# Kernel tuning notes

Hardware: AMD Instinct MI355X
Metric: run time of the kernel (lower is better)

## Reference

```python
import jax, jax.numpy as jnp
import numpy as np

B, S, D = 1, 2048, 1024
H, DH = 16, 64
FF_INNER = 4 * D          # 4096
FUSED = 2 * FF_INNER      # 8192
ROT_BASE = 1000.0


def _rope_tables(seq_len, dim_head):
    # rotarizer: inv_freq = (base ** (arange(0, dh, 2)/dh)) ** -1 ; cached in bfloat16
    inv_freq = 1.0 / (ROT_BASE ** (jnp.arange(0, dim_head, 2, dtype=jnp.float32) / dim_head))
    t = jnp.arange(seq_len, dtype=jnp.float32)
    freqs = jnp.outer(t, inv_freq)                     # [S, DH/2]
    cos = jnp.cos(freqs).astype(jnp.bfloat16)[None, :, None, :]  # [1,S,1,DH/2]
    sin = jnp.sin(freqs).astype(jnp.bfloat16)[None, :, None, :]
    return cos, sin


def _apply_rope(x, cos, sin):
    d = x.shape[-1] // 2
    x1, x2 = x[..., :d], x[..., d:]
    y1 = x1 * cos + x2 * sin
    y2 = -x1 * sin + x2 * cos
    return jnp.concatenate([y1, y2], axis=-1).astype(x.dtype)


def _l2norm(x):
    # F.normalize(p=2, dim=-1), eps=1e-12
    n = jnp.linalg.norm(x, axis=-1, keepdims=True)
    return x / jnp.maximum(n, 1e-12)


def setup_inputs() -> dict:
    key = jax.random.key(0)
    ks = jax.random.split(key, 12)
    std = 0.02
    inp = {
        "h_states": jax.random.normal(ks[0], (B, S, D), jnp.float32),
        "Wq": jax.random.normal(ks[1], (D, D), jnp.float32) * std,
        "Wk": jax.random.normal(ks[2], (D, D), jnp.float32) * std,
        "Wv": jax.random.normal(ks[3], (D, D), jnp.float32) * std,
        "Wqb": jax.random.normal(ks[4], (D, D), jnp.float32) * std,
        "Wkb": jax.random.normal(ks[5], (D, D), jnp.float32) * std,
        "Wo": jax.random.normal(ks[6], (D, D), jnp.float32) * std,
        "bo": jnp.zeros((D,), jnp.float32),
        "W1": jax.random.normal(ks[7], (D, FUSED), jnp.float32) * std,
        "b1": jnp.zeros((FUSED,), jnp.float32),
        "W2": jax.random.normal(ks[8], (FF_INNER, D), jnp.float32) * std,
        "b2": jnp.zeros((D,), jnp.float32),
        "learnedlambda": jnp.asarray(1.0, jnp.float32),
        # l2normscale init: log(S^2 - S) for training_seqlen S
        "l2normscale": jnp.asarray(np.log(float(S) ** 2 - float(S)), np.float32),
    }
    return inp


def reference(h_states, Wq, Wk, Wv, Wqb, Wkb, Wo, bo, W1, b1, W2, b2, learnedlambda, l2normscale):
    b, s, d = h_states.shape
    scale = DH ** -0.5

    # layerwisenorm: RMSNorm, no affine
    eps = jnp.finfo(h_states.dtype).eps
    x = h_states * jax.lax.rsqrt(jnp.mean(jnp.square(h_states), axis=-1, keepdims=True) + eps)

    # projections -> [B,S,H,DH]
    def proj(W):
        return (x @ W).reshape(b, s, H, DH)
    q, k, v = proj(Wq), proj(Wk), proj(Wv)
    qb, kb = proj(Wqb), proj(Wkb)

    cos, sin = _rope_tables(s, DH)
    # per-head qk-norm (l2norm) then rope; v untouched
    q = _apply_rope(_l2norm(q), cos, sin)
    k = _apply_rope(_l2norm(k), cos, sin)
    qb = _apply_rope(_l2norm(qb), cos, sin)
    kb = _apply_rope(_l2norm(kb), cos, sin)

    causal = jnp.tril(jnp.ones((s, s), bool))  # [S,S]

    # main attention: scale=1 (l2norm path), causal softmax, scaled by l2normscale
    scores = jnp.einsum("bqhd,bkhd->bhqk", q, k)
    scores = jnp.where(causal[None, None], scores, -jnp.inf)
    attn = jax.nn.softmax(scores, axis=-1)
    y = l2normscale * jnp.einsum("bhqk,bkhd->bhqd", attn, v)  # [B,H,S,DH]

    # bias attention: masked raw scores @ ones == causal row-sum, broadcast over DH
    sb = jnp.einsum("bqhd,bkhd->bhqk", qb, kb) * scale
    sb = jnp.where(causal[None, None], sb, 0.0)
    y = y + jnp.sum(sb, axis=-1, keepdims=True)  # broadcast over head dim

    y = y.transpose(0, 2, 1, 3).reshape(b, s, d)
    attn_out = y @ Wo + bo

    # fused SwiGLU: chunk -> (x_part, gate); silu(gate) * x_part
    u = x @ W1 + b1
    xp, gate = u[..., :FF_INNER], u[..., FF_INNER:]
    ff = (jax.nn.silu(gate) * xp) @ W2 + b2

    return h_states * learnedlambda + ff + attn_out
```

## Files before the change

kernel.cpp:

```cpp
#include <hip/hip_runtime.h>
#include <hip/hip_bf16.h>
#include <math.h>

typedef __bf16 bf16x8 __attribute__((ext_vector_type(8)));
typedef float  f32x4  __attribute__((ext_vector_type(4)));

#define GLD16(g, l) __builtin_amdgcn_global_load_lds(                      \
    (const __attribute__((address_space(1))) void*)(g),                    \
    (__attribute__((address_space(3))) void*)(l), 16, 0, 0)

#define SCHED_FENCE() __builtin_amdgcn_sched_barrier(0)


__global__ __launch_bounds__(256) void repack_k(
    const float* __restrict__ Wq, const float* __restrict__ Wk,
    const float* __restrict__ Wv, const float* __restrict__ Wqb,
    const float* __restrict__ Wkb, const float* __restrict__ Wo,
    const float* __restrict__ W2, const float* __restrict__ W1,
    __bf16* __restrict__ Wt5, __bf16* __restrict__ WoW2t,
    __bf16* __restrict__ W1t) {
  int t = blockIdx.x;
  const float* in; __bf16* outp;
  int ldin, ldout, r0, c0, cin0, oofs;
  if (t < 5120) {
    int w = t >> 10, rem = t & 1023;
    const float* src[5] = {Wq, Wk, Wv, Wqb, Wkb};
    in = src[w]; ldin = 1024;
    r0 = (rem >> 5) << 5; c0 = (rem & 31) << 5; cin0 = c0;
    outp = Wt5 + (size_t)w * 1048576; ldout = 1024; oofs = 0;
  } else if (t < 6144) {
    int rem = t - 5120;
    in = Wo; ldin = 1024;
    r0 = (rem >> 5) << 5; c0 = (rem & 31) << 5; cin0 = c0;
    outp = WoW2t; ldout = 5120; oofs = 0;
  } else if (t < 10240) {
    int rem = t - 6144;
    in = W2; ldin = 1024;
    r0 = (rem >> 5) << 5; c0 = (rem & 31) << 5; cin0 = c0;
    outp = WoW2t; ldout = 5120; oofs = 1024;
  } else {
    int rem = t - 10240;
    in = W1; ldin = 8192;
    c0 = (rem & 255) << 5; r0 = (rem >> 8) << 5;
    cin0 = ((c0 >> 5) & 1) * 4096 + (c0 >> 6) * 32;
    outp = W1t; ldout = 1024; oofs = 0;
  }
  __shared__ float sh[32][33];
  int tid = threadIdx.x, tx = tid & 31, ty = tid >> 5;
  #pragma unroll
  for (int i = ty; i < 32; i += 8)
    sh[i][tx] = in[(size_t)(r0 + i) * ldin + cin0 + tx];
  __syncthreads();
  #pragma unroll
  for (int i = ty; i < 32; i += 8)
    outp[(size_t)(c0 + i) * ldout + oofs + r0 + tx] = (__bf16)sh[tx][i];
}

__global__ __launch_bounds__(256) void tconv_k(const float* __restrict__ in,
                                               __bf16* __restrict__ out,
                                               int ldin, int ldout) {
  __shared__ float t[32][33];
  int r0 = blockIdx.y * 32, c0 = blockIdx.x * 32;
  int tid = threadIdx.x, tx = tid & 31, ty = tid >> 5;
  #pragma unroll
  for (int i = ty; i < 32; i += 8)
    t[i][tx] = in[(size_t)(r0 + i) * ldin + c0 + tx];
  __syncthreads();
  #pragma unroll
  for (int i = ty; i < 32; i += 8)
    out[(size_t)(c0 + i) * ldout + r0 + tx] = (__bf16)t[tx][i];
}

__global__ __launch_bounds__(256) void rmsnorm_k(const float* __restrict__ hs,
                                                 __bf16* __restrict__ x) {
  int row = blockIdx.x, tid = threadIdx.x;
  const float4 v = ((const float4*)(hs + (size_t)row * 1024))[tid];
  float ss = v.x * v.x + v.y * v.y + v.z * v.z + v.w * v.w;
  #pragma unroll
  for (int o = 32; o > 0; o >>= 1) ss += __shfl_xor(ss, o);
  __shared__ float ps[4];
  if ((tid & 63) == 0) ps[tid >> 6] = ss;
  __syncthreads();
  float tot = ps[0] + ps[1] + ps[2] + ps[3];
  float r = rsqrtf(tot * (1.0f / 1024.0f) + 1.1920929e-7f);
  __bf16* xr = x + (size_t)row * 1024 + tid * 4;
  xr[0] = (__bf16)(v.x * r); xr[1] = (__bf16)(v.y * r);
  xr[2] = (__bf16)(v.z * r); xr[3] = (__bf16)(v.w * r);
}

__global__ __launch_bounds__(256, 3) void gemm_qkv_k(
    const __bf16* __restrict__ A, const __bf16* __restrict__ Bt,
    __bf16* __restrict__ qbf, __bf16* __restrict__ kbf,
    float* __restrict__ qb32, float* __restrict__ kb32,
    float* __restrict__ vproj) {
  const int K = 1024;
  __shared__ __bf16 sA[3][128 * 32];
  __shared__ __bf16 sB[3][128 * 32];
  const int tid = threadIdx.x;
  const int lane = tid & 63;
  const int quad = lane >> 4, l16 = lane & 15;
  const int wave = tid >> 6;
  const int waveM = wave >> 1, waveN = wave & 1;
  const int m0 = blockIdx.y * 128, n0 = blockIdx.x * 128;
  const int nk = K >> 5;
  const int rowS = tid >> 2;
  const int kg = ((tid & 3) ^ ((rowS >> 1) & 3)) * 8;
  const __bf16* gA0 = A + (size_t)(m0 + rowS) * K + kg;
  const __bf16* gA1 = gA0 + (size_t)64 * K;
  const __bf16* gB0 = Bt + (size_t)(n0 + rowS) * K + kg;
  const __bf16* gB1 = gB0 + (size_t)64 * K;
  const int lo0 = tid * 8, lo1 = 2048 + tid * 8;

  auto stage = [&](int t) {
    int s = t % 3;
    __bf16* dA = sA[s];
    __bf16* dB = sB[s];
    GLD16(gA0 + t * 32, dA + lo0);
    GLD16(gA1 + t * 32, dA + lo1);
    GLD16(gB0 + t * 32, dB + lo0);
    GLD16(gB1 + t * 32, dB + lo1);
  };
  stage(0); stage(1);

  f32x4 acc[4][4] = {};
  #pragma unroll 1
  for (int i = 0; i < nk; ++i) {
    if (i < nk - 1)
      asm volatile("s_waitcnt vmcnt(4)" ::: "memory");
    else
      asm volatile("s_waitcnt vmcnt(0)" ::: "memory");
    __builtin_amdgcn_s_barrier();
    SCHED_FENCE();
    int cs = i % 3;
    const __bf16* cA = sA[cs];
    const __bf16* cB = sB[cs];
    if (i + 2 < nk) stage(i + 2);
    SCHED_FENCE();
    bf16x8 af[4], bfv[4];
    #pragma unroll
    for (int mt = 0; mt < 4; ++mt) {
      int r = waveM * 64 + mt * 16 + l16;
      af[mt] = *(const bf16x8*)(cA + r * 32 + ((quad ^ ((r >> 1) & 3)) * 8));
    }
    #pragma unroll
    for (int nt = 0; nt < 4; ++nt) {
      int r = waveN * 64 + nt * 16 + l16;
      bfv[nt] = *(const bf16x8*)(cB + r * 32 + ((quad ^ ((r >> 1) & 3)) * 8));
    }
    __builtin_amdgcn_s_setprio(1);
    #pragma unroll
    for (int mt = 0; mt < 4; ++mt)
      #pragma unroll
      for (int nt = 0; nt < 4; ++nt)
        acc[mt][nt] = __builtin_amdgcn_mfma_f32_16x16x32_bf16(af[mt], bfv[nt], acc[mt][nt], 0, 0, 0);
    __builtin_amdgcn_s_setprio(0);
    SCHED_FENCE();
  }

  const int wid = n0 >> 10;
  const int cw0 = (n0 & 1023) + waveN * 64;
  if (wid == 2) {
    #pragma unroll
    for (int mt = 0; mt < 4; ++mt) {
      int row = m0 + waveM * 64 + mt * 16 + quad * 4;
      #pragma unroll
      for (int nt = 0; nt < 4; ++nt) {
        int col = cw0 + nt * 16 + l16;
        #pragma unroll
        for (int r = 0; r < 4; ++r)
          vproj[(size_t)(row + r) * 1024 + col] = acc[mt][nt][r];
      }
    }
  } else {
    const float inv0 = exp2f(-0.31143076f * (float)l16);
    const float inv1 = exp2f(-0.31143076f * (float)(16 + l16));
    #pragma unroll
    for (int mt = 0; mt < 4; ++mt) {
      #pragma unroll
      for (int r = 0; r < 4; ++r) {
        int srow = m0 + waveM * 64 + mt * 16 + quad * 4 + r;
        float a0 = acc[mt][0][r], a1 = acc[mt][1][r];
        float a2 = acc[mt][2][r], a3 = acc[mt][3][r];
        float ss = a0 * a0 + a1 * a1 + a2 * a2 + a3 * a3;
        ss += __shfl_xor(ss, 1); ss += __shfl_xor(ss, 2);
        ss += __shfl_xor(ss, 4); ss += __shfl_xor(ss, 8);
        float yn = 1.0f / fmaxf(sqrtf(ss), 1e-12f);
        float ang0 = (float)srow * inv0;
        float cb0 = (float)(__bf16)__cosf(ang0);
        float sb0 = (float)(__bf16)__sinf(ang0);
        float ang1 = (float)srow * inv1;
        float cb1 = (float)(__bf16)__cosf(ang1);
        float sb1 = (float)(__bf16)__sinf(ang1);
        float y0 = a0 * yn, y1 = a1 * yn, y2 = a2 * yn, y3 = a3 * yn;
        float o0 =  y0 * cb0 + y2 * sb0;
        float o1 =  y1 * cb1 + y3 * sb1;
        float o2 = -y0 * sb0 + y2 * cb0;
        float o3 = -y1 * sb1 + y3 * cb1;
        size_t base = (size_t)srow * 1024 + cw0 + l16;
        if (wid == 0) {
          qbf[base]      = (__bf16)o0; qbf[base + 16] = (__bf16)o1;
          qbf[base + 32] = (__bf16)o2; qbf[base + 48] = (__bf16)o3;
        } else if (wid == 1) {
          kbf[base]      = (__bf16)o0; kbf[base + 16] = (__bf16)o1;
          kbf[base + 32] = (__bf16)o2; kbf[base + 48] = (__bf16)o3;
        } else if (wid == 3) {
          qb32[base]      = o0; qb32[base + 16] = o1;
          qb32[base + 32] = o2; qb32[base + 48] = o3;
        } else {
          kb32[base]      = o0; kb32[base + 16] = o1;
          kb32[base + 32] = o2; kb32[base + 48] = o3;
        }
      }
    }
  }
}

__global__ __launch_bounds__(256, 3) void gemm_partk_k(
    const __bf16* __restrict__ A, const __bf16* __restrict__ Bt,
    float* __restrict__ P, int N, int K) {
  __shared__ __bf16 sA[3][128 * 32];
  __shared__ __bf16 sB[3][128 * 32];
  const int tid = threadIdx.x;
  const int lane = tid & 63;
  const int quad = lane >> 4, l16 = lane & 15;
  const int wave = tid >> 6;
  const int waveM = wave >> 1, waveN = wave & 1;
  const int m0 = blockIdx.y * 128, n0 = blockIdx.x * 128;
  const int kz = blockIdx.z, nz = gridDim.z;
  const int kper = K / nz, kbeg = kz * kper;
  const int nk = kper >> 5;
  const size_t MN = (size_t)gridDim.y * 128 * N;
  float* C = P + (size_t)kz * MN;
  const int rowS = tid >> 2;
  const int kg = ((tid & 3) ^ ((rowS >> 1) & 3)) * 8;
  const __bf16* gA0 = A + (size_t)(m0 + rowS) * K + kbeg + kg;
  const __bf16* gA1 = gA0 + (size_t)64 * K;
  const __bf16* gB0 = Bt + (size_t)(n0 + rowS) * K + kbeg + kg;
  const __bf16* gB1 = gB0 + (size_t)64 * K;
  const int lo0 = tid * 8, lo1 = 2048 + tid * 8;

  auto stage = [&](int t) {
    int s = t % 3;
    __bf16* dA = sA[s];
    __bf16* dB = sB[s];
    GLD16(gA0 + t * 32, dA + lo0);
    GLD16(gA1 + t * 32, dA + lo1);
    GLD16(gB0 + t * 32, dB + lo0);
    GLD16(gB1 + t * 32, dB + lo1);
  };
  stage(0); stage(1);

  f32x4 acc[4][4] = {};
  #pragma unroll 1
  for (int i = 0; i < nk; ++i) {
    if (i < nk - 1)
      asm volatile("s_waitcnt vmcnt(4)" ::: "memory");
    else
      asm volatile("s_waitcnt vmcnt(0)" ::: "memory");
    __builtin_amdgcn_s_barrier();
    SCHED_FENCE();
    int cs = i % 3;
    const __bf16* cA = sA[cs];
    const __bf16* cB = sB[cs];
    if (i + 2 < nk) stage(i + 2);
    SCHED_FENCE();
    bf16x8 af[4], bfv[4];
    #pragma unroll
    for (int mt = 0; mt < 4; ++mt) {
      int r = waveM * 64 + mt * 16 + l16;
      af[mt] = *(const bf16x8*)(cA + r * 32 + ((quad ^ ((r >> 1) & 3)) * 8));
    }
    #pragma unroll
    for (int nt = 0; nt < 4; ++nt) {
      int r = waveN * 64 + nt * 16 + l16;
      bfv[nt] = *(const bf16x8*)(cB + r * 32 + ((quad ^ ((r >> 1) & 3)) * 8));
    }
    __builtin_amdgcn_s_setprio(1);
    #pragma unroll
    for (int mt = 0; mt < 4; ++mt)
      #pragma unroll
      for (int nt = 0; nt < 4; ++nt)
        acc[mt][nt] = __builtin_amdgcn_mfma_f32_16x16x32_bf16(af[mt], bfv[nt], acc[mt][nt], 0, 0, 0);
    __builtin_amdgcn_s_setprio(0);
    SCHED_FENCE();
  }
  #pragma unroll
  for (int mt = 0; mt < 4; ++mt) {
    int row = m0 + waveM * 64 + mt * 16 + quad * 4;
    #pragma unroll
    for (int nt = 0; nt < 4; ++nt) {
      int col = n0 + waveN * 64 + nt * 16 + l16;
      #pragma unroll
      for (int r = 0; r < 4; ++r)
        C[(size_t)(row + r) * N + col] = acc[mt][nt][r];
    }
  }
}

__global__ __launch_bounds__(512, 2) void ffn1silu_k(
    const __bf16* __restrict__ A, const __bf16* __restrict__ W1t,
    const float* __restrict__ b1, __bf16* __restrict__ ffout) {
  __shared__ __bf16 sA[4][256 * 32];
  __shared__ __bf16 sB[4][256 * 32];
  const int tid = threadIdx.x, lane = tid & 63, w = tid >> 6;
  const int quad = lane >> 4, l16 = lane & 15;
  const int wm = w >> 2, wn = w & 3;
  const int m0 = blockIdx.y * 256;
  const int n0p = blockIdx.x * 256;
  const int K = 1024, NKT = 32;
  const int rowS = tid >> 2;
  const int kg = ((tid & 3) ^ ((rowS >> 1) & 3)) * 8;
  const __bf16* gA0 = A + (size_t)(m0 + rowS) * K + kg;
  const __bf16* gA1 = gA0 + (size_t)128 * K;
  const __bf16* gB0 = W1t + (size_t)(n0p + rowS) * K + kg;
  const __bf16* gB1 = gB0 + (size_t)128 * K;
  const int lo0 = tid * 8, lo1 = 4096 + tid * 8;

  f32x4 acc[8][4] = {};

  auto stageA = [&](int t) {
    __bf16* d = sA[t & 3];
    GLD16(gA0 + t * 32, d + lo0);
    GLD16(gA1 + t * 32, d + lo1);
  };
  auto stageB = [&](int t) {
    __bf16* d = sB[t & 3];
    GLD16(gB0 + t * 32, d + lo0);
    GLD16(gB1 + t * 32, d + lo1);
  };

  auto compute_half = [&](const __bf16* cA, const bf16x8* bfr, int half) {
    bf16x8 af[4];
    #pragma unroll
    for (int mt = 0; mt < 4; ++mt) {
      int r = wm * 128 + half * 64 + mt * 16 + l16;
      af[mt] = *(const bf16x8*)(cA + r * 32 + ((quad ^ ((r >> 1) & 3)) * 8));
    }
    __builtin_amdgcn_s_setprio(1);
    #pragma unroll
    for (int mt = 0; mt < 4; ++mt)
      #pragma unroll
      for (int nt = 0; nt < 4; ++nt)
        acc[half * 4 + mt][nt] = __builtin_amdgcn_mfma_f32_16x16x32_bf16(
            af[mt], bfr[nt], acc[half * 4 + mt][nt], 0, 0, 0);
    __builtin_amdgcn_s_setprio(0);
  };

  stageA(0); stageB(0);
  stageA(1); stageB(1);
  stageA(2); stageB(2);

  #pragma unroll 1
  for (int t = 0; t < NKT; ++t) {
    if (t < NKT - 2)
      asm volatile("s_waitcnt vmcnt(8)" ::: "memory");
    else if (t == NKT - 2)
      asm volatile("s_waitcnt vmcnt(4)" ::: "memory");
    else
      asm volatile("s_waitcnt vmcnt(0)" ::: "memory");
    __builtin_amdgcn_s_barrier();
    SCHED_FENCE();
    const __bf16* cA = sA[t & 3];
    const __bf16* cB = sB[t & 3];
    if (t + 3 < NKT) stageA(t + 3);
    SCHED_FENCE();
    bf16x8 bfr[4];
    #pragma unroll
    for (int nt = 0; nt < 4; ++nt) {
      int r = wn * 64 + nt * 16 + l16;
      bfr[nt] = *(const bf16x8*)(cB + r * 32 + ((quad ^ ((r >> 1) & 3)) * 8));
    }
    compute_half(cA, bfr, 0);
    SCHED_FENCE();
    if (t + 3 < NKT) stageB(t + 3);
    SCHED_FENCE();
    compute_half(cA, bfr, 1);
    SCHED_FENCE();
  }

  const int colbase = (blockIdx.x * 4 + wn) * 32;
  #pragma unroll
  for (int j = 0; j < 8; ++j) {
    int row = m0 + wm * 128 + (j >> 2) * 64 + (j & 3) * 16 + quad * 4;
    #pragma unroll
    for (int p = 0; p < 2; ++p) {
      int col = colbase + p * 16 + l16;
      float bxv = b1[col], bgv = b1[col + 4096];
      #pragma unroll
      for (int r = 0; r < 4; ++r) {
        float xp = acc[j][p][r] + bxv;
        float g  = acc[j][p + 2][r] + bgv;
        float val = xp * g / (1.f + __expf(-g));
        ffout[(size_t)(row + r) * 5120 + 1024 + col] = (__bf16)val;
      }
    }
  }
}

__global__ __launch_bounds__(256) void combine_k(
    const float* __restrict__ P, const float* __restrict__ b2,
    const float* __restrict__ bo, const float* __restrict__ hs,
    const float* __restrict__ plam, float* __restrict__ out) {
  const size_t MN = (size_t)2048 * 1024;
  size_t i = ((size_t)blockIdx.x * 256 + threadIdx.x) * 4;
  int col = (int)(i & 1023);
  float4 a0 = *(const float4*)(P + i);
  float4 a1 = *(const float4*)(P + MN + i);
  float4 a2 = *(const float4*)(P + 2 * MN + i);
  float4 a3 = *(const float4*)(P + 3 * MN + i);
  float4 h  = *(const float4*)(hs + i);
  float4 v2 = *(const float4*)(b2 + col);
  float4 vo = *(const float4*)(bo + col);
  float lam = plam[0];
  float4 o;
  o.x = (a0.x + a1.x) + (a2.x + a3.x) + v2.x + vo.x + lam * h.x;
  o.y = (a0.y + a1.y) + (a2.y + a3.y) + v2.y + vo.y + lam * h.y;
  o.z = (a0.z + a1.z) + (a2.z + a3.z) + v2.z + vo.z + lam * h.z;
  o.w = (a0.w + a1.w) + (a2.w + a3.w) + v2.w + vo.w + lam * h.w;
  *(float4*)(out + i) = o;
}

__global__ __launch_bounds__(256) void kbsum_k(const float* __restrict__ kb,
                                               float* __restrict__ tsum,
                                               float* __restrict__ tsum8) {
  int t = blockIdx.x, h = blockIdx.y;
  int d = threadIdx.x & 63, w = threadIdx.x >> 6;
  size_t base = (size_t)h * 64 + d;
  float s = 0.f;
  #pragma unroll
  for (int r = 0; r < 8; ++r)
    s += kb[(size_t)(t * 32 + w * 8 + r) * 1024 + base];
  tsum8[(size_t)((t * 4 + w) * 16 + h) * 64 + d] = s;
  __shared__ float ps[4][64];
  ps[w][d] = s;
  __syncthreads();
  if (w == 0)
    tsum[(size_t)(t * 16 + h) * 64 + d] = (ps[0][d] + ps[1][d]) + (ps[2][d] + ps[3][d]);
}

__global__ __launch_bounds__(256) void sbrow2_k(const float* __restrict__ qb,
                                                const float* __restrict__ kb,
                                                const float* __restrict__ tsum,
                                                const float* __restrict__ tsum8,
                                                float* __restrict__ sb) {
  int t = blockIdx.x, h = blockIdx.y;
  int d = threadIdx.x & 63, g = threadIdx.x >> 6;
  size_t base = (size_t)h * 64 + d;
  float run = 0.f;
  for (int tp = 0; tp < t; ++tp) run += tsum[(size_t)(tp * 16 + h) * 64 + d];
  for (int w = 0; w < g; ++w) run += tsum8[(size_t)((t * 4 + w) * 16 + h) * 64 + d];
  int r0 = t * 32 + g * 8;
  for (int s0 = 0; s0 < 8; s0 += 4) {
    float p[4];
    #pragma unroll
    for (int u = 0; u < 4; ++u) {
      size_t off = (size_t)(r0 + s0 + u) * 1024 + base;
      run += kb[off];
      p[u] = qb[off] * run;
    }
    #pragma unroll
    for (int o = 32; o > 0; o >>= 1) {
      #pragma unroll
      for (int u = 0; u < 4; ++u) p[u] += __shfl_xor(p[u], o);
    }
    if (d == 0) {
      #pragma unroll
      for (int u = 0; u < 4; ++u) sb[(r0 + s0 + u) * 16 + h] = 0.125f * p[u];
    }
  }
}

__global__ __launch_bounds__(256) void attn_k(const __bf16* __restrict__ qg,
    const __bf16* __restrict__ kg, const __bf16* __restrict__ vtg,
    float* __restrict__ o_part, float* __restrict__ l_part) {
  __shared__ __bf16 sK[2][64 * 64];
  __shared__ __bf16 sVt[2][64 * 64];
  __shared__ __bf16 sP[4][16 * 64];
  const int pair = blockIdx.x, j4 = blockIdx.y, hh = blockIdx.z;
  const int tid = threadIdx.x, lane = tid & 63, w = tid >> 6;
  const int quad = lane >> 4, l16 = lane & 15;
  const int srow = tid >> 3;
  const int sg = (tid & 7) ^ (srow & 7);
  __bf16* sPw = sP[w];

  auto stage = [&](int kt) {
    int b = kt & 1;
    const __bf16* gK = kg + (size_t)(kt * 64 + srow) * 1024 + hh * 64 + sg * 8;
    const __bf16* gV = vtg + (size_t)(hh * 64 + srow) * 2048 + kt * 64 + sg * 8;
    GLD16(gK, sK[b] + tid * 8);
    GLD16(gK + (size_t)32 * 1024, sK[b] + tid * 8 + 2048);
    GLD16(gV, sVt[b] + tid * 8);
    GLD16(gV + (size_t)32 * 2048, sVt[b] + tid * 8 + 2048);
  };

  for (int phase = 0; phase < 2; ++phase) {
    const int qt = phase ? 31 - pair : pair;
    const int q0 = qt * 64;
    const int n = qt + 1;
    const int kb = (j4 * n) >> 2, ke = ((j4 + 1) * n) >> 2;
    bf16x8 qf[2];
    #pragma unroll
    for (int kk = 0; kk < 2; ++kk)
      qf[kk] = *(const bf16x8*)(qg + (size_t)(q0 + w * 16 + l16) * 1024 + hh * 64 + kk * 32 + quad * 8);
    f32x4 accO[4] = {};
    float l_[4] = {0.f, 0.f, 0.f, 0.f};

    __syncthreads();
    if (kb < ke) stage(kb);

    for (int kt = kb; kt < ke; ++kt) {
      __syncthreads();
      SCHED_FENCE();
      if (kt + 1 < ke) stage(kt + 1);
      SCHED_FENCE();
      const __bf16* cK = sK[kt & 1];
      const __bf16* cV = sVt[kt & 1];

      f32x4 s4[4];
      #pragma unroll
      for (int nt = 0; nt < 4; ++nt) {
        int r = nt * 16 + l16;
        bf16x8 b0 = *(const bf16x8*)(cK + r * 64 + ((quad ^ (r & 7)) * 8));
        bf16x8 b1 = *(const bf16x8*)(cK + r * 64 + (((4 + quad) ^ (r & 7)) * 8));
        f32x4 sa = {0.f, 0.f, 0.f, 0.f};
        sa = __builtin_amdgcn_mfma_f32_16x16x32_bf16(qf[0], b0, sa, 0, 0, 0);
        sa = __builtin_amdgcn_mfma_f32_16x16x32_bf16(qf[1], b1, sa, 0, 0, 0);
        s4[nt] = sa;
      }
      if (kt == qt) {
        #pragma unroll
        for (int nt = 0; nt < 4; ++nt)
          #pragma unroll
          for (int r = 0; r < 4; ++r)
            if (nt * 16 + l16 > w * 16 + quad * 4 + r) s4[nt][r] = -INFINITY;
      }
      float p[4][4];
      #pragma unroll
      for (int nt = 0; nt < 4; ++nt)
        #pragma unroll
        for (int r = 0; r < 4; ++r)
          p[nt][r] = __expf(s4[nt][r] - 1.0f);
      #pragma unroll
      for (int r = 0; r < 4; ++r)
        l_[r] += (p[0][r] + p[1][r]) + (p[2][r] + p[3][r]);
      #pragma unroll
      for (int nt = 0; nt < 4; ++nt)
        #pragma unroll
        for (int r = 0; r < 4; ++r) {
          int row = quad * 4 + r, col = nt * 16 + l16;
          sPw[row * 64 + (col ^ ((row & 7) << 3))] = (__bf16)p[nt][r];
        }
      #pragma unroll
      for (int kk = 0; kk < 2; ++kk) {
        bf16x8 a = *(const bf16x8*)(sPw + l16 * 64 + (((kk * 4 + quad) ^ (l16 & 7)) * 8));
        #pragma unroll
        for (int nt = 0; nt < 4; ++nt) {
          int vr = nt * 16 + l16;
          bf16x8 bv = *(const bf16x8*)(cV + vr * 64 + (((kk * 4 + quad) ^ (vr & 7)) * 8));
          accO[nt] = __builtin_amdgcn_mfma_f32_16x16x32_bf16(a, bv, accO[nt], 0, 0, 0);
        }
      }
    }
    #pragma unroll
    for (int o = 1; o < 16; o <<= 1)
      #pragma unroll
      for (int r = 0; r < 4; ++r) l_[r] += __shfl_xor(l_[r], o);
    #pragma unroll
    for (int r = 0; r < 4; ++r) {
      int grow = q0 + w * 16 + quad * 4 + r;
      if (l16 == 0)
        l_part[((size_t)j4 * 2048 + grow) * 16 + hh] = l_[r];
      #pragma unroll
      for (int nt = 0; nt < 4; ++nt)
        o_part[((size_t)j4 * 2048 + grow) * 1024 + hh * 64 + nt * 16 + l16] = accO[nt][r];
    }
  }
}

__global__ __launch_bounds__(256) void attnmerge_k(const float* __restrict__ o_part,
    const float* __restrict__ l_part, const float* __restrict__ sbr,
    const float* __restrict__ pl2s, __bf16* __restrict__ yo) {
  int idx = blockIdx.x * 256 + threadIdx.x;
  int s = idx >> 8, rem = idx & 255;
  int h = rem >> 4, dg = (rem & 15) * 4;
  float den = 0.f;
  float4 acc = {0.f, 0.f, 0.f, 0.f};
  #pragma unroll
  for (int j = 0; j < 4; ++j) {
    den += l_part[((size_t)j * 2048 + s) * 16 + h];
    float4 o = *(const float4*)(o_part + ((size_t)j * 2048 + s) * 1024 + h * 64 + dg);
    acc.x += o.x; acc.y += o.y; acc.z += o.z; acc.w += o.w;
  }
  float sc = pl2s[0] / den;
  float add = sbr[s * 16 + h];
  __bf16* yp = yo + (size_t)s * 5120 + h * 64 + dg;
  yp[0] = (__bf16)(sc * acc.x + add);
  yp[1] = (__bf16)(sc * acc.y + add);
  yp[2] = (__bf16)(sc * acc.z + add);
  yp[3] = (__bf16)(sc * acc.w + add);
}

extern "C" void kernel_launch(void* const* d_in, const int* in_sizes, int n_in,
                              void* d_out, int out_size, void* d_ws, size_t ws_size,
                              hipStream_t stream) {
  (void)in_sizes; (void)n_in; (void)out_size; (void)ws_size;
  const float* hs   = (const float*)d_in[0];
  const float* Wq   = (const float*)d_in[1];
  const float* Wk   = (const float*)d_in[2];
  const float* Wv   = (const float*)d_in[3];
  const float* Wqb  = (const float*)d_in[4];
  const float* Wkb  = (const float*)d_in[5];
  const float* Wo   = (const float*)d_in[6];
  const float* bo   = (const float*)d_in[7];
  const float* W1   = (const float*)d_in[8];
  const float* b1   = (const float*)d_in[9];
  const float* W2   = (const float*)d_in[10];
  const float* b2   = (const float*)d_in[11];
  const float* plam = (const float*)d_in[12];
  const float* pl2s = (const float*)d_in[13];
  float* out = (float*)d_out;
  char* ws = (char*)d_ws;

  size_t off = 0;
  auto alloc = [&](size_t bytes) { char* p = ws + off; off += (bytes + 255) & ~(size_t)255; return p; };
  __bf16* Wt5    = (__bf16*)alloc((size_t)5 * 1024 * 1024 * 2);
  __bf16* WoW2t  = (__bf16*)alloc((size_t)1024 * 5120 * 2);
  __bf16* W1t    = (__bf16*)alloc((size_t)8192 * 1024 * 2);
  __bf16* xbf    = (__bf16*)alloc((size_t)2048 * 1024 * 2);
  __bf16* concat = (__bf16*)alloc((size_t)2048 * 5120 * 2);
  float*  proj  = (float*)alloc((size_t)2048 * 5120 * 4);
  float*  qbf32 = (float*)alloc((size_t)2048 * 1024 * 4);
  float*  kbf32 = (float*)alloc((size_t)2048 * 1024 * 4);
  __bf16* qbf   = (__bf16*)alloc((size_t)2048 * 1024 * 2);
  __bf16* kbf   = (__bf16*)alloc((size_t)2048 * 1024 * 2);
  float*  vproj  = proj;
  float*  o_part = proj;
  float*  l_part = qbf32;
  float*  gpart  = proj;
  __bf16* vtbf  = (__bf16*)alloc((size_t)1024 * 2048 * 2);
  float*  sbrow = (float*)alloc((size_t)2048 * 16 * 4);
  float*  tsum  = (float*)alloc((size_t)64 * 16 * 64 * 4);
  float*  tsum8 = (float*)alloc((size_t)256 * 16 * 64 * 4);

  repack_k<<<18432, 256, 0, stream>>>(Wq, Wk, Wv, Wqb, Wkb, Wo, W2, W1,
                                      Wt5, WoW2t, W1t);

  rmsnorm_k<<<2048, 256, 0, stream>>>(hs, xbf);
  gemm_qkv_k<<<dim3(40, 16), 256, 0, stream>>>(xbf, Wt5, qbf, kbf,
                                               qbf32, kbf32, vproj);
  tconv_k<<<dim3(32, 64), 256, 0, stream>>>(vproj, vtbf, 1024, 2048);
  kbsum_k<<<dim3(64, 16), 256, 0, stream>>>(kbf32, tsum, tsum8);
  sbrow2_k<<<dim3(64, 16), 256, 0, stream>>>(qbf32, kbf32, tsum, tsum8, sbrow);
  attn_k<<<dim3(16, 4, 16), 256, 0, stream>>>(qbf, kbf, vtbf, o_part, l_part);
  attnmerge_k<<<2048, 256, 0, stream>>>(o_part, l_part, sbrow, pl2s, concat);
  ffn1silu_k<<<dim3(32, 8), 512, 0, stream>>>(xbf, W1t, b1, concat);
  gemm_partk_k<<<dim3(8, 16, 4), 256, 0, stream>>>(concat, WoW2t, gpart, 1024, 5120);
  combine_k<<<2048, 256, 0, stream>>>(gpart, b2, bo, hs, plam, out);
}
```

Before: 333.4 us.

## Fuse V transpose into QKV GEMM epilogue and split GEMM K-loop into staged halves

The QKV GEMM now writes V directly as transposed bf16 (vtbf) in its epilogue, which removes the separate tconv kernel and the fp32 vproj round trip. The K-loops of the QKV GEMM, the partial-K GEMM and the FFN1 GEMM are restructured so that the A and B tile prefetches are issued separately. Each half of the MFMA work is preceded by its own LDS fragment loads plus an extra barrier and lgkmcnt wait. This is meant to interleave global-to-LDS copies with compute, at the cost of more barriers per iteration. The transposed epilogue stores are strided 8-byte writes, which may coalesce poorly.

New measurement: 326.0 us (median of 2 runs). -2.2%, faster.

```diff
diff --git a/kernel.cpp b/kernel.cpp
--- a/kernel.cpp
+++ b/kernel.cpp
@@ -3,6 +3,7 @@
 #include <math.h>
 
 typedef __bf16 bf16x8 __attribute__((ext_vector_type(8)));
+typedef __bf16 bf16x4 __attribute__((ext_vector_type(4)));
 typedef float  f32x4  __attribute__((ext_vector_type(4)));
 
 #define GLD16(g, l) __builtin_amdgcn_global_load_lds(                      \
@@ -56,21 +57,6 @@
     outp[(size_t)(c0 + i) * ldout + oofs + r0 + tx] = (__bf16)sh[tx][i];
 }
 
-__global__ __launch_bounds__(256) void tconv_k(const float* __restrict__ in,
-                                               __bf16* __restrict__ out,
-                                               int ldin, int ldout) {
-  __shared__ float t[32][33];
-  int r0 = blockIdx.y * 32, c0 = blockIdx.x * 32;
-  int tid = threadIdx.x, tx = tid & 31, ty = tid >> 5;
-  #pragma unroll
-  for (int i = ty; i < 32; i += 8)
-    t[i][tx] = in[(size_t)(r0 + i) * ldin + c0 + tx];
-  __syncthreads();
-  #pragma unroll
-  for (int i = ty; i < 32; i += 8)
-    out[(size_t)(c0 + i) * ldout + r0 + tx] = (__bf16)t[tx][i];
-}
-
 __global__ __launch_bounds__(256) void rmsnorm_k(const float* __restrict__ hs,
                                                  __bf16* __restrict__ x) {
   int row = blockIdx.x, tid = threadIdx.x;
@@ -92,7 +78,7 @@
     const __bf16* __restrict__ A, const __bf16* __restrict__ Bt,
     __bf16* __restrict__ qbf, __bf16* __restrict__ kbf,
     float* __restrict__ qb32, float* __restrict__ kb32,
-    float* __restrict__ vproj) {
+    __bf16* __restrict__ vtbf) {
   const int K = 1024;
   __shared__ __bf16 sA[3][128 * 32];
   __shared__ __bf16 sB[3][128 * 32];
@@ -111,16 +97,18 @@
   const __bf16* gB1 = gB0 + (size_t)64 * K;
   const int lo0 = tid * 8, lo1 = 2048 + tid * 8;
 
-  auto stage = [&](int t) {
-    int s = t % 3;
-    __bf16* dA = sA[s];
-    __bf16* dB = sB[s];
+  auto stageA = [&](int t) {
+    __bf16* dA = sA[t % 3];
     GLD16(gA0 + t * 32, dA + lo0);
     GLD16(gA1 + t * 32, dA + lo1);
+  };
+  auto stageB = [&](int t) {
+    __bf16* dB = sB[t % 3];
     GLD16(gB0 + t * 32, dB + lo0);
     GLD16(gB1 + t * 32, dB + lo1);
   };
-  stage(0); stage(1);
+  stageA(0); stageB(0);
+  stageA(1); stageB(1);
 
   f32x4 acc[4][4] = {};
   #pragma unroll 1
@@ -131,25 +119,45 @@
       asm volatile("s_waitcnt vmcnt(0)" ::: "memory");
     __builtin_amdgcn_s_barrier();
     SCHED_FENCE();
-    int cs = i % 3;
-    const __bf16* cA = sA[cs];
-    const __bf16* cB = sB[cs];
-    if (i + 2 < nk) stage(i + 2);
-    SCHED_FENCE();
+    const __bf16* cA = sA[i % 3];
+    const __bf16* cB = sB[i % 3];
     bf16x8 af[4], bfv[4];
-    #pragma unroll
-    for (int mt = 0; mt < 4; ++mt) {
-      int r = waveM * 64 + mt * 16 + l16;
-      af[mt] = *(const bf16x8*)(cA + r * 32 + ((quad ^ ((r >> 1) & 3)) * 8));
-    }
     #pragma unroll
     for (int nt = 0; nt < 4; ++nt) {
       int r = waveN * 64 + nt * 16 + l16;
       bfv[nt] = *(const bf16x8*)(cB + r * 32 + ((quad ^ ((r >> 1) & 3)) * 8));
     }
+    #pragma unroll
+    for (int mt = 0; mt < 2; ++mt) {
+      int r = waveM * 64 + mt * 16 + l16;
+      af[mt] = *(const bf16x8*)(cA + r * 32 + ((quad ^ ((r >> 1) & 3)) * 8));
+    }
+    if (i + 2 < nk) stageA(i + 2);
+    SCHED_FENCE();
+    __builtin_amdgcn_s_barrier();
+    asm volatile("s_waitcnt lgkmcnt(0)" ::: "memory");
+    SCHED_FENCE();
     __builtin_amdgcn_s_setprio(1);
     #pragma unroll
-    for (int mt = 0; mt < 4; ++mt)
+    for (int mt = 0; mt < 2; ++mt)
+      #pragma unroll
+      for (int nt = 0; nt < 4; ++nt)
+        acc[mt][nt] = __builtin_amdgcn_mfma_f32_16x16x32_bf16(af[mt], bfv[nt], acc[mt][nt], 0, 0, 0);
+    __builtin_amdgcn_s_setprio(0);
+    SCHED_FENCE();
+    #pragma unroll
+    for (int mt = 2; mt < 4; ++mt) {
+      int r = waveM * 64 + mt * 16 + l16;
+      af[mt] = *(const bf16x8*)(cA + r * 32 + ((quad ^ ((r >> 1) & 3)) * 8));
+    }
+    if (i + 2 < nk) stageB(i + 2);
+    SCHED_FENCE();
+    __builtin_amdgcn_s_barrier();
+    asm volatile("s_waitcnt lgkmcnt(0)" ::: "memory");
+    SCHED_FENCE();
+    __builtin_amdgcn_s_setprio(1);
+    #pragma unroll
+    for (int mt = 2; mt < 4; ++mt)
       #pragma unroll
       for (int nt = 0; nt < 4; ++nt)
         acc[mt][nt] = __builtin_amdgcn_mfma_f32_16x16x32_bf16(af[mt], bfv[nt], acc[mt][nt], 0, 0, 0);
@@ -166,9 +174,10 @@
       #pragma unroll
       for (int nt = 0; nt < 4; ++nt) {
         int col = cw0 + nt * 16 + l16;
-        #pragma unroll
-        for (int r = 0; r < 4; ++r)
-          vproj[(size_t)(row + r) * 1024 + col] = acc[mt][nt][r];
+        bf16x4 v;
+        v[0] = (__bf16)acc[mt][nt][0]; v[1] = (__bf16)acc[mt][nt][1];
+        v[2] = (__bf16)acc[mt][nt][2]; v[3] = (__bf16)acc[mt][nt][3];
+        *(bf16x4*)(vtbf + (size_t)col * 2048 + row) = v;
       }
     }
   } else {
@@ -239,16 +248,18 @@
   const __bf16* gB1 = gB0 + (size_t)64 * K;
   const int lo0 = tid * 8, lo1 = 2048 + tid * 8;
 
-  auto stage = [&](int t) {
-    int s = t % 3;
-    __bf16* dA = sA[s];
-    __bf16* dB = sB[s];
+  auto stageA = [&](int t) {
+    __bf16* dA = sA[t % 3];
     GLD16(gA0 + t * 32, dA + lo0);
     GLD16(gA1 + t * 32, dA + lo1);
+  };
+  auto stageB = [&](int t) {
+    __bf16* dB = sB[t % 3];
     GLD16(gB0 + t * 32, dB + lo0);
     GLD16(gB1 + t * 32, dB + lo1);
   };
-  stage(0); stage(1);
+  stageA(0); stageB(0);
+  stageA(1); stageB(1);
 
   f32x4 acc[4][4] = {};
   #pragma unroll 1
@@ -259,25 +270,45 @@
       asm volatile("s_waitcnt vmcnt(0)" ::: "memory");
     __builtin_amdgcn_s_barrier();
     SCHED_FENCE();
-    int cs = i % 3;
-    const __bf16* cA = sA[cs];
-    const __bf16* cB = sB[cs];
-    if (i + 2 < nk) stage(i + 2);
-    SCHED_FENCE();
+    const __bf16* cA = sA[i % 3];
+    const __bf16* cB = sB[i % 3];
     bf16x8 af[4], bfv[4];
-    #pragma unroll
-    for (int mt = 0; mt < 4; ++mt) {
-      int r = waveM * 64 + mt * 16 + l16;
-      af[mt] = *(const bf16x8*)(cA + r * 32 + ((quad ^ ((r >> 1) & 3)) * 8));
-    }
     #pragma unroll
     for (int nt = 0; nt < 4; ++nt) {
       int r = waveN * 64 + nt * 16 + l16;
       bfv[nt] = *(const bf16x8*)(cB + r * 32 + ((quad ^ ((r >> 1) & 3)) * 8));
     }
+    #pragma unroll
+    for (int mt = 0; mt < 2; ++mt) {
+      int r = waveM * 64 + mt * 16 + l16;
+      af[mt] = *(const bf16x8*)(cA + r * 32 + ((quad ^ ((r >> 1) & 3)) * 8));
+    }
+    if (i + 2 < nk) stageA(i + 2);
+    SCHED_FENCE();
+    __builtin_amdgcn_s_barrier();
+    asm volatile("s_waitcnt lgkmcnt(0)" ::: "memory");
+    SCHED_FENCE();
     __builtin_amdgcn_s_setprio(1);
     #pragma unroll
-    for (int mt = 0; mt < 4; ++mt)
+    for (int mt = 0; mt < 2; ++mt)
+      #pragma unroll
+      for (int nt = 0; nt < 4; ++nt)
+        acc[mt][nt] = __builtin_amdgcn_mfma_f32_16x16x32_bf16(af[mt], bfv[nt], acc[mt][nt], 0, 0, 0);
+    __builtin_amdgcn_s_setprio(0);
+    SCHED_FENCE();
+    #pragma unroll
+    for (int mt = 2; mt < 4; ++mt) {
+      int r = waveM * 64 + mt * 16 + l16;
+      af[mt] = *(const bf16x8*)(cA + r * 32 + ((quad ^ ((r >> 1) & 3)) * 8));
+    }
+    if (i + 2 < nk) stageB(i + 2);
+    SCHED_FENCE();
+    __builtin_amdgcn_s_barrier();
+    asm volatile("s_waitcnt lgkmcnt(0)" ::: "memory");
+    SCHED_FENCE();
+    __builtin_amdgcn_s_setprio(1);
+    #pragma unroll
+    for (int mt = 2; mt < 4; ++mt)
       #pragma unroll
       for (int nt = 0; nt < 4; ++nt)
         acc[mt][nt] = __builtin_amdgcn_mfma_f32_16x16x32_bf16(af[mt], bfv[nt], acc[mt][nt], 0, 0, 0);
@@ -329,23 +360,6 @@
     GLD16(gB1 + t * 32, d + lo1);
   };
 
-  auto compute_half = [&](const __bf16* cA, const bf16x8* bfr, int half) {
-    bf16x8 af[4];
-    #pragma unroll
-    for (int mt = 0; mt < 4; ++mt) {
-      int r = wm * 128 + half * 64 + mt * 16 + l16;
-      af[mt] = *(const bf16x8*)(cA + r * 32 + ((quad ^ ((r >> 1) & 3)) * 8));
-    }
-    __builtin_amdgcn_s_setprio(1);
-    #pragma unroll
-    for (int mt = 0; mt < 4; ++mt)
-      #pragma unroll
-      for (int nt = 0; nt < 4; ++nt)
-        acc[half * 4 + mt][nt] = __builtin_amdgcn_mfma_f32_16x16x32_bf16(
-            af[mt], bfr[nt], acc[half * 4 + mt][nt], 0, 0, 0);
-    __builtin_amdgcn_s_setprio(0);
-  };
-
   stageA(0); stageB(0);
   stageA(1); stageB(1);
   stageA(2); stageB(2);
@@ -362,19 +376,48 @@
     SCHED_FENCE();
     const __bf16* cA = sA[t & 3];
     const __bf16* cB = sB[t & 3];
-    if (t + 3 < NKT) stageA(t + 3);
-    SCHED_FENCE();
-    bf16x8 bfr[4];
+    bf16x8 bfr[4], af[4];
     #pragma unroll
     for (int nt = 0; nt < 4; ++nt) {
       int r = wn * 64 + nt * 16 + l16;
       bfr[nt] = *(const bf16x8*)(cB + r * 32 + ((quad ^ ((r >> 1) & 3)) * 8));
     }
-    compute_half(cA, bfr, 0);
-    SCHED_FENCE();
+    #pragma unroll
+    for (int mt = 0; mt < 4; ++mt) {
+      int r = wm * 128 + mt * 16 + l16;
+      af[mt] = *(const bf16x8*)(cA + r * 32 + ((quad ^ ((r >> 1) & 3)) * 8));
+    }
+    if (t + 3 < NKT) stageA(t + 3);
+    SCHED_FENCE();
+    __builtin_amdgcn_s_barrier();
+    asm volatile("s_waitcnt lgkmcnt(0)" ::: "memory");
+    SCHED_FENCE();
+    __builtin_amdgcn_s_setprio(1);
+    #pragma unroll
+    for (int mt = 0; mt < 4; ++mt)
+      #pragma unroll
+      for (int nt = 0; nt < 4; ++nt)
+        acc[mt][nt] = __builtin_amdgcn_mfma_f32_16x16x32_bf16(af[mt], bfr[nt], acc[mt][nt], 0, 0, 0);
+    __builtin_amdgcn_s_setprio(0);
+    SCHED_FENCE();
+    bf16x8 af1[4];
+    #pragma unroll
+    for (int mt = 0; mt < 4; ++mt) {
+      int r = wm * 128 + 64 + mt * 16 + l16;
+      af1[mt] = *(const bf16x8*)(cA + r * 32 + ((quad ^ ((r >> 1) & 3)) * 8));
+    }
     if (t + 3 < NKT) stageB(t + 3);
     SCHED_FENCE();
-    compute_half(cA, bfr, 1);
+    __builtin_amdgcn_s_barrier();
+    asm volatile("s_waitcnt lgkmcnt(0)" ::: "memory");
+    SCHED_FENCE();
+    __builtin_amdgcn_s_setprio(1);
+    #pragma unroll
+    for (int mt = 0; mt < 4; ++mt)
+      #pragma unroll
+      for (int nt = 0; nt < 4; ++nt)
+        acc[4 + mt][nt] = __builtin_amdgcn_mfma_f32_16x16x32_bf16(af1[mt], bfr[nt], acc[4 + mt][nt], 0, 0, 0);
+    __builtin_amdgcn_s_setprio(0);
     SCHED_FENCE();
   }
 
@@ -633,7 +676,6 @@
   float*  kbf32 = (float*)alloc((size_t)2048 * 1024 * 4);
   __bf16* qbf   = (__bf16*)alloc((size_t)2048 * 1024 * 2);
   __bf16* kbf   = (__bf16*)alloc((size_t)2048 * 1024 * 2);
-  float*  vproj  = proj;
   float*  o_part = proj;
   float*  l_part = qbf32;
   float*  gpart  = proj;
@@ -647,8 +689,7 @@
 
   rmsnorm_k<<<2048, 256, 0, stream>>>(hs, xbf);
   gemm_qkv_k<<<dim3(40, 16), 256, 0, stream>>>(xbf, Wt5, qbf, kbf,
-                                               qbf32, kbf32, vproj);
-  tconv_k<<<dim3(32, 64), 256, 0, stream>>>(vproj, vtbf, 1024, 2048);
+                                               qbf32, kbf32, vtbf);
   kbsum_k<<<dim3(64, 16), 256, 0, stream>>>(kbf32, tsum, tsum8);
   sbrow2_k<<<dim3(64, 16), 256, 0, stream>>>(qbf32, kbf32, tsum, tsum8, sbrow);
   attn_k<<<dim3(16, 4, 16), 256, 0, stream>>>(qbf, kbf, vtbf, o_part, l_part);
```
